# Kernel optimization log

Measured on AMD Instinct MI355X. Metric: run time of the kernel, lower is better.

Reference implementation:

```python
import jax, jax.numpy as jnp
import numpy as np
import math

EPS_NORM = 1e-12   # F.normalize eps
EPS_LN = 1e-5      # F.layer_norm default eps
EPS_STD = 1e-6     # hierarchical_norm spatial eps


def _l2_normalize(x, axis):
    n = jnp.linalg.norm(x, axis=axis, keepdims=True)
    return x / jnp.maximum(n, EPS_NORM)


def setup_inputs() -> dict:
    key = jax.random.key(0)
    k1, k2, k3, k4, k5 = jax.random.split(key, 5)
    B, C, H, W, D, L = 512, 256, 14, 14, 512, 196
    return {
        "image_features": jax.random.normal(k1, (B, D), jnp.float32),
        "text_features": jax.random.normal(k2, (B, D), jnp.float32),
        "sam_features": jax.random.normal(k3, (B, C, H, W), jnp.float32),
        "W_sim": jax.random.normal(k4, (L, D), jnp.float32) * 0.02,
        "b_sim": jax.random.normal(k5, (L,), jnp.float32) * 0.02,
    }


def reference(image_features, text_features, sam_features, W_sim, b_sim):
    B, C, H, W = sam_features.shape
    L = H * W

    # L2 normalize CLIP features
    imf = _l2_normalize(image_features, axis=1)   # (B, 512)
    txt = _l2_normalize(text_features, axis=1)    # (B, 512)

    # dynamic_similarity
    cross_attn = jnp.einsum('bc,bc->b', imf, txt)                 # (B,)
    spatial_weights = jax.nn.sigmoid(imf @ W_sim.T + b_sim)       # (B, L)
    similarity_weights = cross_attn[:, None] * spatial_weights / 10.0  # (B, L)

    # spatial self-attention over SAM features
    sam_flat = sam_features.reshape(B, C, L)                      # (B, C, L)
    sam_norm = _l2_normalize(sam_flat, axis=1)
    scores = jnp.einsum('bcl,bcm->blm', sam_norm, sam_norm) / math.sqrt(C)
    attn = jax.nn.softmax(scores, axis=-1)                        # (B, L, L)
    weighted = jnp.einsum('bcl,blm->bcm', sam_flat, attn)         # (B, C, L)

    combined = (sam_flat + weighted) * 0.5
    guide = combined * similarity_weights[:, None, :]             # (B, C, L)
    x = guide.reshape(B, C, H, W)

    # hierarchical_norm: LayerNorm over channel dim (no affine), then spatial standardization
    mu_c = x.mean(axis=1, keepdims=True)
    var_c = x.var(axis=1, keepdims=True)  # biased, matches F.layer_norm
    x = (x - mu_c) / jnp.sqrt(var_c + EPS_LN)
    sp_mean = x.mean(axis=(2, 3), keepdims=True)
    sp_std = jnp.std(x, axis=(2, 3), keepdims=True, ddof=1)  # torch .std() uses Bessel correction
    return (x - sp_mean) / (sp_std + EPS_STD)
```

## Files before the change

### kernel.cpp

```cpp
#include <hip/hip_runtime.h>
#include <math.h>


typedef float f32x4 __attribute__((ext_vector_type(4)));
typedef short s16x8 __attribute__((ext_vector_type(8)));

__device__ __forceinline__ float wsum(float v) {
#pragma unroll
  for (int o = 32; o > 0; o >>= 1) v += __shfl_xor(v, o, 64);
  return v;
}

__device__ __forceinline__ unsigned short f2bf(float f) {
  unsigned int u = __float_as_uint(f);
  u += 0x7FFFu + ((u >> 16) & 1u);
  return (unsigned short)(u >> 16);
}

__device__ __forceinline__ s16x8 pack8(f32x4 lo, f32x4 hi) {
  s16x8 r;
  r[0] = (short)f2bf(lo[0]);
  r[1] = (short)f2bf(lo[1]);
  r[2] = (short)f2bf(lo[2]);
  r[3] = (short)f2bf(lo[3]);
  r[4] = (short)f2bf(hi[0]);
  r[5] = (short)f2bf(hi[1]);
  r[6] = (short)f2bf(hi[2]);
  r[7] = (short)f2bf(hi[3]);
  return r;
}

__global__ __launch_bounds__(256) void k_simw(const float* __restrict__ img,
                                              const float* __restrict__ txt,
                                              const float* __restrict__ Wsim,
                                              const float* __restrict__ bsim,
                                              float* __restrict__ simw) {
  const int b = blockIdx.x, tid = threadIdx.x, lane = tid & 63, wv = tid >> 6;
  __shared__ float s_img[512];
  __shared__ float s_part[3][4];

  float i0 = img[b * 512 + tid], i1 = img[b * 512 + 256 + tid];
  float t0 = txt[b * 512 + tid], t1 = txt[b * 512 + 256 + tid];
  float ssi = wsum(i0 * i0 + i1 * i1);
  float sst = wsum(t0 * t0 + t1 * t1);
  float dd = wsum(i0 * t0 + i1 * t1);
  if (lane == 0) { s_part[0][wv] = ssi; s_part[1][wv] = sst; s_part[2][wv] = dd; }
  __syncthreads();
  float ni = fmaxf(sqrtf(s_part[0][0] + s_part[0][1] + s_part[0][2] + s_part[0][3]), 1e-12f);
  float nt = fmaxf(sqrtf(s_part[1][0] + s_part[1][1] + s_part[1][2] + s_part[1][3]), 1e-12f);
  float dot = s_part[2][0] + s_part[2][1] + s_part[2][2] + s_part[2][3];
  float cross = dot / (ni * nt);
  float rni = 1.0f / ni;
  s_img[tid] = i0 * rni;
  s_img[tid + 256] = i1 * rni;
  __syncthreads();

  for (int l = wv; l < 196; l += 4) {
    const float* wr = Wsim + (size_t)l * 512;
    float p = 0.f;
#pragma unroll
    for (int k = 0; k < 8; ++k) p = fmaf(s_img[lane + 64 * k], wr[lane + 64 * k], p);
    p = wsum(p);
    if (lane == 0) {
      float z = p + bsim[l];
      float sg = 1.0f / (1.0f + __expf(-z));
      simw[b * 196 + l] = cross * sg * 0.1f;
    }
  }
}

__global__ __launch_bounds__(256) void k_prep(const float* __restrict__ sam,
                                              unsigned short* __restrict__ samnT) {
  const int b = blockIdx.x, tid = threadIdx.x, lane = tid & 63, wv = tid >> 6;
  const float* __restrict__ S = sam + (size_t)b * 50176;
  unsigned short* __restrict__ NT = samnT + (size_t)b * (208 * 256);
  __shared__ float s_inv[196];
  __shared__ float T[64 * 197];

  if (tid < 196) {
    float ss = 0.f;
    for (int c = 0; c < 256; ++c) {
      float v = S[c * 196 + tid];
      ss = fmaf(v, v, ss);
    }
    s_inv[tid] = 1.0f / fmaxf(sqrtf(ss), 1e-12f);
  }
  for (int i = tid; i < 1536; i += 256) ((unsigned int*)(NT + 196 * 256))[i] = 0;
  __syncthreads();

  for (int c0 = 0; c0 < 256; c0 += 64) {
    for (int cr = wv; cr < 64; cr += 4) {
      const float* Sr = S + (c0 + cr) * 196;
      float* Tr = T + cr * 197;
      Tr[lane] = Sr[lane] * s_inv[lane];
      Tr[lane + 64] = Sr[lane + 64] * s_inv[lane + 64];
      Tr[lane + 128] = Sr[lane + 128] * s_inv[lane + 128];
      if (lane < 4) Tr[lane + 192] = Sr[lane + 192] * s_inv[lane + 192];
    }
    __syncthreads();
    const int lrow = tid >> 3, cch = tid & 7;
    for (int l0 = 0; l0 < 196; l0 += 32) {
      int l = l0 + lrow;
      if (l < 196) {
        const float* Tc = T + (cch * 8) * 197 + l;
        unsigned short r[8];
#pragma unroll
        for (int k = 0; k < 8; ++k) r[k] = f2bf(Tc[k * 197]);
        uint4 o;
        o.x = r[0] | ((unsigned int)r[1] << 16);
        o.y = r[2] | ((unsigned int)r[3] << 16);
        o.z = r[4] | ((unsigned int)r[5] << 16);
        o.w = r[6] | ((unsigned int)r[7] << 16);
        *(uint4*)(NT + l * 256 + c0 + cch * 8) = o;
      }
    }
    __syncthreads();
  }
}

__device__ __forceinline__ void proc_strip(int s, f32x4* sc, unsigned short* AT,
                                           int quad, int l15) {
  const bool mval12 = (192 + l15) < 196;
  float mx[4], rs[4];
#pragma unroll
  for (int r = 0; r < 4; ++r) {
    float m = -3e38f;
#pragma unroll
    for (int j = 0; j < 13; ++j) {
      float v = sc[j][r];
      if (j == 12 && !mval12) v = -3e38f;
      m = fmaxf(m, v);
    }
#pragma unroll
    for (int o = 1; o < 16; o <<= 1) m = fmaxf(m, __shfl_xor(m, o, 64));
    float s_ = 0.f;
#pragma unroll
    for (int j = 0; j < 13; ++j) {
      float e = __expf(sc[j][r] - m);
      if (j == 12 && !mval12) e = 0.f;
      s_ += e;
    }
#pragma unroll
    for (int o = 1; o < 16; o <<= 1) s_ += __shfl_xor(s_, o, 64);
    mx[r] = m;
    rs[r] = 1.0f / s_;
  }
  const int lb = s * 16 + quad * 4;
#pragma unroll
  for (int j = 0; j < 13; ++j) {
    unsigned short u[4];
#pragma unroll
    for (int r = 0; r < 4; ++r) {
      float a = __expf(sc[j][r] - mx[r]) * rs[r];
      if (lb + r >= 196) a = 0.f;
      u[r] = f2bf(a);
    }
    uint2 o2;
    o2.x = u[0] | ((unsigned int)u[1] << 16);
    o2.y = u[2] | ((unsigned int)u[3] << 16);
    *(uint2*)(AT + (j * 16 + l15) * 224 + lb) = o2;
  }
}

__global__ __launch_bounds__(256, 2) void k_scores(const unsigned short* __restrict__ samnT,
                                                   unsigned short* __restrict__ attnT) {
  const int b = blockIdx.x, tid = threadIdx.x, lane = tid & 63, wv = tid >> 6;
  const int quad = lane >> 4, l15 = lane & 15;
  const unsigned short* __restrict__ NT = samnT + (size_t)b * (208 * 256);
  unsigned short* __restrict__ AT = attnT + (size_t)b * (208 * 224);
  __shared__ unsigned short sN[208 * 136];

  for (int i = tid; i < 208 * 8; i += 256) {
    int m = i >> 3, k = i & 7;
    ((unsigned int*)(AT + m * 224 + 208))[k] = 0;
  }

  for (int pr = 0; pr < 2; ++pr) {
    const int p = wv + 4 * pr;
    const int s0 = 2 * p, s1 = (2 * p + 1 < 13) ? (2 * p + 1) : 12;
    f32x4 sc0[13], sc1[13];
    const f32x4 z = {0.f, 0.f, 0.f, 0.f};
#pragma unroll
    for (int j = 0; j < 13; ++j) { sc0[j] = z; sc1[j] = z; }
    for (int h = 0; h < 2; ++h) {
      __syncthreads();
      for (int i = tid; i < 208 * 16; i += 256) {
        int l = i >> 4, cc = i & 15;
        *(uint4*)(sN + l * 136 + cc * 8) = *(const uint4*)(NT + l * 256 + h * 128 + cc * 8);
      }
      __syncthreads();
      if (p < 7) {
        s16x8 A0[4], A1[4];
#pragma unroll
        for (int ct = 0; ct < 4; ++ct) {
          A0[ct] = *(const s16x8*)(sN + (s0 * 16 + l15) * 136 + ct * 32 + quad * 8);
          A1[ct] = *(const s16x8*)(sN + (s1 * 16 + l15) * 136 + ct * 32 + quad * 8);
        }
#pragma unroll
        for (int j = 0; j < 13; ++j) {
#pragma unroll
          for (int ct = 0; ct < 4; ++ct) {
            s16x8 Bf = *(const s16x8*)(sN + (j * 16 + l15) * 136 + ct * 32 + quad * 8);
            sc0[j] = __builtin_amdgcn_mfma_f32_16x16x32_bf16(A0[ct], Bf, sc0[j], 0, 0, 0);
            sc1[j] = __builtin_amdgcn_mfma_f32_16x16x32_bf16(A1[ct], Bf, sc1[j], 0, 0, 0);
          }
        }
      }
    }
    if (p < 7) {
      proc_strip(s0, sc0, AT, quad, l15);
      proc_strip(s1, sc1, AT, quad, l15);
    }
  }
}

__global__ __launch_bounds__(256, 4) void k_weighted2(const float* __restrict__ sam,
                                                      const unsigned short* __restrict__ attnT,
                                                      const float* __restrict__ simw,
                                                      float* __restrict__ out) {
  const int b = blockIdx.x, q = blockIdx.y;
  const int tid = threadIdx.x, lane = tid & 63, wv = tid >> 6;
  const int quad = lane >> 4, l15 = lane & 15;
  const float* __restrict__ S = sam + (size_t)b * 50176;
  const unsigned short* __restrict__ AT = attnT + (size_t)b * (208 * 224);
  float* __restrict__ O = out + (size_t)b * 50176;
  const int cbase = q * 64 + wv * 16;

  __shared__ float tile[4][8 * 196];

  f32x4 acc[13];
  const f32x4 z4 = {0.f, 0.f, 0.f, 0.f};
#pragma unroll
  for (int mb = 0; mb < 13; ++mb) acc[mb] = z4;

  const float* __restrict__ Sa = S + (size_t)(cbase + l15) * 196;
  const unsigned short* __restrict__ Bp = AT + l15 * 224 + quad * 8;

#pragma unroll
  for (int kt = 0; kt < 7; ++kt) {
    s16x8 A;
    if (kt < 6) {
      const float* p = Sa + kt * 32 + quad * 8;
      A = pack8(*(const f32x4*)p, *(const f32x4*)(p + 4));
    } else {
      f32x4 lo = z4;
      if (quad == 0) lo = *(const f32x4*)(Sa + 192);
      A = pack8(lo, z4);
    }
    const unsigned short* Bk = Bp + kt * 32;
#pragma unroll
    for (int mb = 0; mb < 13; ++mb) {
      s16x8 Bf = *(const s16x8*)(Bk + mb * 16 * 224);
      acc[mb] = __builtin_amdgcn_mfma_f32_16x16x32_bf16(A, Bf, acc[mb], 0, 0, 0);
    }
  }

  float wj0 = simw[b * 196 + lane] * 0.5f;
  float wj1 = simw[b * 196 + 64 + lane] * 0.5f;
  float wj2 = simw[b * 196 + 128 + lane] * 0.5f;
  float wj3 = 0.f;
  if (lane < 4) wj3 = simw[b * 196 + 192 + lane] * 0.5f;

  float* tl = &tile[wv][0];
  for (int half = 0; half < 2; ++half) {
    if ((quad >> 1) == half) {
      const int qq = quad & 1;
#pragma unroll
      for (int mb = 0; mb < 13; ++mb) {
        const int m = mb * 16 + l15;
        if (m < 196) {
#pragma unroll
          for (int r = 0; r < 4; ++r) tl[(qq * 4 + r) * 196 + m] = acc[mb][r];
        }
      }
    }
    __syncthreads();
    const int rowg0 = cbase + half * 8;
#pragma unroll
    for (int rr = 0; rr < 8; ++rr) {
      const float* trow = tl + rr * 196;
      const float* Sr = S + (size_t)(rowg0 + rr) * 196;
      float* Or = O + (size_t)(rowg0 + rr) * 196;
      Or[lane] = (Sr[lane] + trow[lane]) * wj0;
      Or[lane + 64] = (Sr[lane + 64] + trow[lane + 64]) * wj1;
      Or[lane + 128] = (Sr[lane + 128] + trow[lane + 128]) * wj2;
      if (lane < 4) Or[lane + 192] = (Sr[lane + 192] + trow[lane + 192]) * wj3;
    }
    __syncthreads();
  }
}

__global__ __launch_bounds__(256) void k_attn(const float* __restrict__ sam,
                                              const float* __restrict__ simw,
                                              float* __restrict__ out) {
  const int b = blockIdx.x;
  const int tid = threadIdx.x, lane = tid & 63, wv = tid >> 6;
  const float* __restrict__ S = sam + (size_t)b * (256 * 196);
  float* __restrict__ O = out + (size_t)b * (256 * 196);
  const float* __restrict__ SW = simw + b * 196;

  __shared__ float s_inv[196];
  __shared__ float s_max[196];
  __shared__ float s_rsum[196];
  __shared__ float bufS[28 * 197];
  __shared__ float bufT[256 * 29];

  for (int l = tid; l < 196; l += 256) {
    float ss = 0.f;
    for (int c = 0; c < 256; ++c) {
      float v = S[c * 196 + l];
      ss = fmaf(v, v, ss);
    }
    s_inv[l] = 1.0f / fmaxf(sqrtf(ss), 1e-12f);
  }

  for (int r0 = 0; r0 < 196; r0 += 28) {
    float acc[7][4];
#pragma unroll
    for (int i = 0; i < 7; ++i)
#pragma unroll
      for (int j = 0; j < 4; ++j) acc[i][j] = 0.f;
    const int lr = r0 + wv * 7;
    for (int ct = 0; ct < 8; ++ct) {
      __syncthreads();
      for (int i = tid; i < 32 * 196; i += 256)
        bufT[(i / 196) * 197 + (i % 196)] = S[ct * 32 * 196 + i];
      __syncthreads();
#pragma unroll 2
      for (int c = 0; c < 32; ++c) {
        const float* row = bufT + c * 197;
        float a[7];
#pragma unroll
        for (int i = 0; i < 7; ++i) a[i] = row[lr + i];
        float b0 = row[lane], b1 = row[lane + 64], b2 = row[lane + 128];
        float b3 = row[lane + 192];
#pragma unroll
        for (int i = 0; i < 7; ++i) {
          acc[i][0] = fmaf(a[i], b0, acc[i][0]);
          acc[i][1] = fmaf(a[i], b1, acc[i][1]);
          acc[i][2] = fmaf(a[i], b2, acc[i][2]);
          acc[i][3] = fmaf(a[i], b3, acc[i][3]);
        }
      }
    }
#pragma unroll
    for (int j = 0; j < 4; ++j) {
      int m = lane + 64 * j;
      if (m < 196) {
        float im = s_inv[m] * 0.0625f;
#pragma unroll
        for (int i = 0; i < 7; ++i)
          bufS[(wv * 7 + i) * 197 + m] = acc[i][j] * s_inv[lr + i] * im;
      }
    }
    __syncthreads();
#pragma unroll
    for (int i = 0; i < 7; ++i) {
      const int rl = wv * 7 + i;
      const float* sr = bufS + rl * 197;
      float v0 = sr[lane], v1 = sr[lane + 64], v2 = sr[lane + 128];
      bool g = (lane + 192) < 196;
      float v3 = g ? sr[lane + 192] : -1e30f;
      float mxv = fmaxf(fmaxf(v0, v1), fmaxf(v2, v3));
#pragma unroll
      for (int o = 32; o > 0; o >>= 1) mxv = fmaxf(mxv, __shfl_xor(mxv, o, 64));
      float sm = __expf(v0 - mxv) + __expf(v1 - mxv) + __expf(v2 - mxv) +
                 (g ? __expf(v3 - mxv) : 0.f);
      sm = wsum(sm);
      if (lane == 0) { s_max[r0 + rl] = mxv; s_rsum[r0 + rl] = 1.0f / sm; }
    }
  }
  __syncthreads();

  const int cg = tid >> 2, tq = tid & 3;
  for (int m0 = 0; m0 < 196; m0 += 28) {
    float acc[7][4];
#pragma unroll
    for (int i = 0; i < 7; ++i)
#pragma unroll
      for (int j = 0; j < 4; ++j) acc[i][j] = 0.f;
    const int mg = m0 + wv * 7;
    for (int ct = 0; ct < 8; ++ct) {
      __syncthreads();
      for (int i = tid; i < 32 * 196; i += 256)
        bufT[(i / 196) * 197 + (i % 196)] = S[ct * 32 * 196 + i];
      __syncthreads();
#pragma unroll 2
      for (int c = 0; c < 32; ++c) {
        const float* row = bufT + c * 197;
        float a[7];
#pragma unroll
        for (int i = 0; i < 7; ++i) a[i] = row[mg + i];
        float b0 = row[lane], b1 = row[lane + 64], b2 = row[lane + 128];
        float b3 = row[lane + 192];
#pragma unroll
        for (int i = 0; i < 7; ++i) {
          acc[i][0] = fmaf(a[i], b0, acc[i][0]);
          acc[i][1] = fmaf(a[i], b1, acc[i][1]);
          acc[i][2] = fmaf(a[i], b2, acc[i][2]);
          acc[i][3] = fmaf(a[i], b3, acc[i][3]);
        }
      }
    }
    __syncthreads();
#pragma unroll
    for (int j = 0; j < 4; ++j) {
      int l = lane + 64 * j;
      if (l < 196) {
        float il = s_inv[l] * 0.0625f;
        float mxl = s_max[l], rsl = s_rsum[l];
#pragma unroll
        for (int i = 0; i < 7; ++i) {
          float sc = acc[i][j] * s_inv[mg + i] * il;
          bufS[(wv * 7 + i) * 197 + l] = __expf(sc - mxl) * rsl;
        }
      }
    }
    __syncthreads();
    float w[4][7];
#pragma unroll
    for (int ii = 0; ii < 4; ++ii)
#pragma unroll
      for (int i = 0; i < 7; ++i) w[ii][i] = 0.f;
    for (int lt = 0; lt < 7; ++lt) {
      __syncthreads();
      for (int i = tid; i < 256 * 28; i += 256) {
        int c = i / 28, j = i - c * 28;
        bufT[c * 29 + j] = S[c * 196 + lt * 28 + j];
      }
      __syncthreads();
#pragma unroll 4
      for (int j = 0; j < 28; ++j) {
        float a0 = bufT[(cg * 4 + 0) * 29 + j];
        float a1 = bufT[(cg * 4 + 1) * 29 + j];
        float a2 = bufT[(cg * 4 + 2) * 29 + j];
        float a3 = bufT[(cg * 4 + 3) * 29 + j];
#pragma unroll
        for (int i = 0; i < 7; ++i) {
          float bv = bufS[(tq * 7 + i) * 197 + lt * 28 + j];
          w[0][i] = fmaf(a0, bv, w[0][i]);
          w[1][i] = fmaf(a1, bv, w[1][i]);
          w[2][i] = fmaf(a2, bv, w[2][i]);
          w[3][i] = fmaf(a3, bv, w[3][i]);
        }
      }
    }
#pragma unroll
    for (int i = 0; i < 7; ++i) {
      const int m = m0 + tq * 7 + i;
      float sw = SW[m] * 0.5f;
#pragma unroll
      for (int ii = 0; ii < 4; ++ii) {
        const int c = cg * 4 + ii;
        O[c * 196 + m] = (S[c * 196 + m] + w[ii][i]) * sw;
      }
    }
  }
}

__global__ __launch_bounds__(256) void k_norm(float* __restrict__ x) {
  const int b = blockIdx.x, tid = threadIdx.x;
  float* __restrict__ X = x + (size_t)b * (256 * 196);
  __shared__ float s_mu[196], s_rs[196];
  __shared__ float s_rm[256], s_rc[256];
  __shared__ float tile[256 * 29];

  if (tid < 196) {
    float s = 0.f, q = 0.f;
    for (int c = 0; c < 256; ++c) {
      float v = X[c * 196 + tid];
      s += v;
      q = fmaf(v, v, q);
    }
    float mu = s * (1.0f / 256.0f);
    float var = q * (1.0f / 256.0f) - mu * mu;
    s_mu[tid] = mu;
    s_rs[tid] = rsqrtf(fmaxf(var, 0.f) + 1e-5f);
  }
  __syncthreads();

  float rs = 0.f, rq = 0.f;
  for (int m0 = 0; m0 < 196; m0 += 28) {
    __syncthreads();
    for (int i = tid; i < 256 * 28; i += 256) {
      int c = i / 28, j = i - c * 28;
      tile[c * 29 + j] = X[c * 196 + m0 + j];
    }
    __syncthreads();
#pragma unroll
    for (int j = 0; j < 28; ++j) {
      float y = (tile[tid * 29 + j] - s_mu[m0 + j]) * s_rs[m0 + j];
      rs += y;
      rq = fmaf(y, y, rq);
    }
  }
  float rm = rs * (1.0f / 196.0f);
  float var = (rq - 196.0f * rm * rm) * (1.0f / 195.0f);
  float sd = sqrtf(fmaxf(var, 0.f));
  s_rm[tid] = rm;
  s_rc[tid] = 1.0f / (sd + 1e-6f);
  __syncthreads();

  for (int i = tid; i < 256 * 196; i += 256) {
    int c = i / 196, m = i - c * 196;
    float y = (X[i] - s_mu[m]) * s_rs[m];
    X[i] = (y - s_rm[c]) * s_rc[c];
  }
}

extern "C" void kernel_launch(void* const* d_in, const int* in_sizes, int n_in,
                              void* d_out, int out_size, void* d_ws, size_t ws_size,
                              hipStream_t stream) {
  const float* img = (const float*)d_in[0];
  const float* txt = (const float*)d_in[1];
  const float* sam = (const float*)d_in[2];
  const float* Wsim = (const float*)d_in[3];
  const float* bsim = (const float*)d_in[4];
  float* out = (float*)d_out;

  const int B = in_sizes[0] / 512;

  const size_t simw_bytes = (((size_t)B * 196 * 4) + 511) & ~(size_t)511;
  const size_t samnT_bytes = (size_t)B * 208 * 256 * 2;
  const size_t attnT_bytes = (size_t)B * 208 * 224 * 2;
  const size_t need = simw_bytes + samnT_bytes + attnT_bytes;

  float* simw = (float*)d_ws;

  k_simw<<<B, 256, 0, stream>>>(img, txt, Wsim, bsim, simw);

  if (ws_size >= need) {
    unsigned short* samnT = (unsigned short*)((char*)d_ws + simw_bytes);
    unsigned short* attnT = (unsigned short*)((char*)d_ws + simw_bytes + samnT_bytes);
    k_prep<<<B, 256, 0, stream>>>(sam, samnT);
    k_scores<<<B, 256, 0, stream>>>(samnT, attnT);
    k_weighted2<<<dim3(B, 4), 256, 0, stream>>>(sam, attnT, simw, out);
  } else {
    k_attn<<<B, 256, 0, stream>>>(sam, simw, out);
  }
  k_norm<<<B, 256, 0, stream>>>(out);
}
```

Baseline: 471.6 us.

## Split score kernel into per-strip wavefront blocks and fuse channel stats into weighted pass

Replaces the block-per-batch score kernel with one 64-thread block per 16-row strip. These blocks read operands straight from global memory (L2-friendly, XCD-aware ordering) instead of staging through LDS with barriers. The weighted kernel now also produces per-position channel sums and sums of squares, so the new normalization kernel skips one statistics pass over the output and splits each batch across two blocks. Padding zeroing moves into the prep kernel. Risks include more redundant global/L2 reads of B operands and single-pass variance precision.

```diff
diff --git a/kernel.cpp b/kernel.cpp
--- a/kernel.cpp
+++ b/kernel.cpp
@@ -70,12 +70,19 @@
 }
 
 __global__ __launch_bounds__(256) void k_prep(const float* __restrict__ sam,
-                                              unsigned short* __restrict__ samnT) {
+                                              unsigned short* __restrict__ samnT,
+                                              unsigned short* __restrict__ attnT) {
   const int b = blockIdx.x, tid = threadIdx.x, lane = tid & 63, wv = tid >> 6;
   const float* __restrict__ S = sam + (size_t)b * 50176;
   unsigned short* __restrict__ NT = samnT + (size_t)b * (208 * 256);
+  unsigned short* __restrict__ ATz = attnT + (size_t)b * (208 * 224);
   __shared__ float s_inv[196];
   __shared__ float T[64 * 197];
+
+  for (int i = tid; i < 208 * 8; i += 256) {
+    int m = i >> 3, k = i & 7;
+    ((unsigned int*)(ATz + m * 224 + 208))[k] = 0;
+  }
 
   if (tid < 196) {
     float ss = 0.f;
@@ -162,62 +169,51 @@
   }
 }
 
-__global__ __launch_bounds__(256, 2) void k_scores(const unsigned short* __restrict__ samnT,
-                                                   unsigned short* __restrict__ attnT) {
-  const int b = blockIdx.x, tid = threadIdx.x, lane = tid & 63, wv = tid >> 6;
-  const int quad = lane >> 4, l15 = lane & 15;
+__global__ __launch_bounds__(64) void k_scores2(const unsigned short* __restrict__ samnT,
+                                                unsigned short* __restrict__ attnT) {
+  int id = blockIdx.x;
+  int b, s;
+  if (gridDim.x == 512 * 13) {
+    int x = id & 7, j = id >> 3;
+    int bb = j / 13;
+    b = x * 64 + bb;
+    s = j - bb * 13;
+  } else {
+    int bb = id / 13;
+    b = bb;
+    s = id - bb * 13;
+  }
+  const int lane = threadIdx.x, quad = lane >> 4, l15 = lane & 15;
   const unsigned short* __restrict__ NT = samnT + (size_t)b * (208 * 256);
   unsigned short* __restrict__ AT = attnT + (size_t)b * (208 * 224);
-  __shared__ unsigned short sN[208 * 136];
-
-  for (int i = tid; i < 208 * 8; i += 256) {
-    int m = i >> 3, k = i & 7;
-    ((unsigned int*)(AT + m * 224 + 208))[k] = 0;
-  }
-
-  for (int pr = 0; pr < 2; ++pr) {
-    const int p = wv + 4 * pr;
-    const int s0 = 2 * p, s1 = (2 * p + 1 < 13) ? (2 * p + 1) : 12;
-    f32x4 sc0[13], sc1[13];
-    const f32x4 z = {0.f, 0.f, 0.f, 0.f};
-#pragma unroll
-    for (int j = 0; j < 13; ++j) { sc0[j] = z; sc1[j] = z; }
-    for (int h = 0; h < 2; ++h) {
-      __syncthreads();
-      for (int i = tid; i < 208 * 16; i += 256) {
-        int l = i >> 4, cc = i & 15;
-        *(uint4*)(sN + l * 136 + cc * 8) = *(const uint4*)(NT + l * 256 + h * 128 + cc * 8);
-      }
-      __syncthreads();
-      if (p < 7) {
-        s16x8 A0[4], A1[4];
-#pragma unroll
-        for (int ct = 0; ct < 4; ++ct) {
-          A0[ct] = *(const s16x8*)(sN + (s0 * 16 + l15) * 136 + ct * 32 + quad * 8);
-          A1[ct] = *(const s16x8*)(sN + (s1 * 16 + l15) * 136 + ct * 32 + quad * 8);
-        }
-#pragma unroll
-        for (int j = 0; j < 13; ++j) {
-#pragma unroll
-          for (int ct = 0; ct < 4; ++ct) {
-            s16x8 Bf = *(const s16x8*)(sN + (j * 16 + l15) * 136 + ct * 32 + quad * 8);
-            sc0[j] = __builtin_amdgcn_mfma_f32_16x16x32_bf16(A0[ct], Bf, sc0[j], 0, 0, 0);
-            sc1[j] = __builtin_amdgcn_mfma_f32_16x16x32_bf16(A1[ct], Bf, sc1[j], 0, 0, 0);
-          }
-        }
-      }
-    }
-    if (p < 7) {
-      proc_strip(s0, sc0, AT, quad, l15);
-      proc_strip(s1, sc1, AT, quad, l15);
-    }
-  }
+
+  s16x8 A[8];
+  const unsigned short* Ar = NT + (s * 16 + l15) * 256 + quad * 8;
+#pragma unroll
+  for (int ct = 0; ct < 8; ++ct) A[ct] = *(const s16x8*)(Ar + ct * 32);
+
+  f32x4 sc[13];
+  const f32x4 z = {0.f, 0.f, 0.f, 0.f};
+#pragma unroll
+  for (int j = 0; j < 13; ++j) sc[j] = z;
+
+#pragma unroll
+  for (int j = 0; j < 13; ++j) {
+    const unsigned short* Br = NT + (j * 16 + l15) * 256 + quad * 8;
+#pragma unroll
+    for (int ct = 0; ct < 8; ++ct) {
+      s16x8 Bf = *(const s16x8*)(Br + ct * 32);
+      sc[j] = __builtin_amdgcn_mfma_f32_16x16x32_bf16(A[ct], Bf, sc[j], 0, 0, 0);
+    }
+  }
+  proc_strip(s, sc, AT, quad, l15);
 }
 
 __global__ __launch_bounds__(256, 4) void k_weighted2(const float* __restrict__ sam,
                                                       const unsigned short* __restrict__ attnT,
                                                       const float* __restrict__ simw,
-                                                      float* __restrict__ out) {
+                                                      float* __restrict__ out,
+                                                      float* __restrict__ stats) {
   const int b = blockIdx.x, q = blockIdx.y;
   const int tid = threadIdx.x, lane = tid & 63, wv = tid >> 6;
   const int quad = lane >> 4, l15 = lane & 15;
@@ -261,6 +257,9 @@
   float wj3 = 0.f;
   if (lane < 4) wj3 = simw[b * 196 + 192 + lane] * 0.5f;
 
+  float st0 = 0.f, st1 = 0.f, st2 = 0.f, st3 = 0.f;
+  float sq0 = 0.f, sq1 = 0.f, sq2 = 0.f, sq3 = 0.f;
+
   float* tl = &tile[wv][0];
   for (int half = 0; half < 2; ++half) {
     if ((quad >> 1) == half) {
@@ -281,10 +280,82 @@
       const float* trow = tl + rr * 196;
       const float* Sr = S + (size_t)(rowg0 + rr) * 196;
       float* Or = O + (size_t)(rowg0 + rr) * 196;
-      Or[lane] = (Sr[lane] + trow[lane]) * wj0;
-      Or[lane + 64] = (Sr[lane + 64] + trow[lane + 64]) * wj1;
-      Or[lane + 128] = (Sr[lane + 128] + trow[lane + 128]) * wj2;
-      if (lane < 4) Or[lane + 192] = (Sr[lane + 192] + trow[lane + 192]) * wj3;
+      float v0 = (Sr[lane] + trow[lane]) * wj0;
+      float v1 = (Sr[lane + 64] + trow[lane + 64]) * wj1;
+      float v2 = (Sr[lane + 128] + trow[lane + 128]) * wj2;
+      Or[lane] = v0;
+      Or[lane + 64] = v1;
+      Or[lane + 128] = v2;
+      st0 += v0; sq0 = fmaf(v0, v0, sq0);
+      st1 += v1; sq1 = fmaf(v1, v1, sq1);
+      st2 += v2; sq2 = fmaf(v2, v2, sq2);
+      if (lane < 4) {
+        float v3 = (Sr[lane + 192] + trow[lane + 192]) * wj3;
+        Or[lane + 192] = v3;
+        st3 += v3; sq3 = fmaf(v3, v3, sq3);
+      }
+    }
+    __syncthreads();
+  }
+
+  tl[lane] = st0; tl[lane + 64] = st1; tl[lane + 128] = st2;
+  if (lane < 4) tl[lane + 192] = st3;
+  tl[784 + lane] = sq0; tl[784 + lane + 64] = sq1; tl[784 + lane + 128] = sq2;
+  if (lane < 4) tl[784 + lane + 192] = sq3;
+  __syncthreads();
+  if (tid < 196) {
+    float s = tile[0][tid] + tile[1][tid] + tile[2][tid] + tile[3][tid];
+    float qsum = tile[0][784 + tid] + tile[1][784 + tid] + tile[2][784 + tid] + tile[3][784 + tid];
+    stats[((size_t)(b * 4 + q) * 2 + 0) * 196 + tid] = s;
+    stats[((size_t)(b * 4 + q) * 2 + 1) * 196 + tid] = qsum;
+  }
+}
+
+__global__ __launch_bounds__(256) void k_norm2(float* __restrict__ x,
+                                               const float* __restrict__ stats) {
+  const int b = blockIdx.x, q = blockIdx.y, tid = threadIdx.x;
+  float* __restrict__ X = x + (size_t)b * 50176 + (size_t)q * 128 * 196;
+  __shared__ float s_mu[196], s_rs[196];
+  __shared__ float s_rm[32], s_rc[32];
+  __shared__ float T[32][197];
+
+  if (tid < 196) {
+    const float* st = stats + (size_t)b * 8 * 196;
+    float s = st[tid] + st[2 * 196 + tid] + st[4 * 196 + tid] + st[6 * 196 + tid];
+    float sq = st[196 + tid] + st[3 * 196 + tid] + st[5 * 196 + tid] + st[7 * 196 + tid];
+    float mu = s * (1.0f / 256.0f);
+    float var = sq * (1.0f / 256.0f) - mu * mu;
+    s_mu[tid] = mu;
+    s_rs[tid] = rsqrtf(fmaxf(var, 0.f) + 1e-5f);
+  }
+  __syncthreads();
+
+  for (int rg = 0; rg < 4; ++rg) {
+    float* Xg = X + rg * 32 * 196;
+    for (int i = tid; i < 32 * 196; i += 256) T[i / 196][i % 196] = Xg[i];
+    __syncthreads();
+    const int r = tid >> 3, p = tid & 7;
+    float ys = 0.f, yq = 0.f;
+    for (int m = p; m < 196; m += 8) {
+      float y = (T[r][m] - s_mu[m]) * s_rs[m];
+      ys += y;
+      yq = fmaf(y, y, yq);
+    }
+    ys += __shfl_xor(ys, 1, 64); yq += __shfl_xor(yq, 1, 64);
+    ys += __shfl_xor(ys, 2, 64); yq += __shfl_xor(yq, 2, 64);
+    ys += __shfl_xor(ys, 4, 64); yq += __shfl_xor(yq, 4, 64);
+    if (p == 0) {
+      float rm = ys * (1.0f / 196.0f);
+      float var = (yq - 196.0f * rm * rm) * (1.0f / 195.0f);
+      float sd = sqrtf(fmaxf(var, 0.f));
+      s_rm[r] = rm;
+      s_rc[r] = 1.0f / (sd + 1e-6f);
+    }
+    __syncthreads();
+    for (int i = tid; i < 32 * 196; i += 256) {
+      int rr = i / 196, m = i % 196;
+      float y = (T[rr][m] - s_mu[m]) * s_rs[m];
+      Xg[i] = (y - s_rm[rr]) * s_rc[rr];
     }
     __syncthreads();
   }
@@ -523,7 +594,8 @@
   const size_t simw_bytes = (((size_t)B * 196 * 4) + 511) & ~(size_t)511;
   const size_t samnT_bytes = (size_t)B * 208 * 256 * 2;
   const size_t attnT_bytes = (size_t)B * 208 * 224 * 2;
-  const size_t need = simw_bytes + samnT_bytes + attnT_bytes;
+  const size_t stats_bytes = (size_t)B * 4 * 2 * 196 * 4;
+  const size_t need = simw_bytes + samnT_bytes + attnT_bytes + stats_bytes;
 
   float* simw = (float*)d_ws;
 
@@ -532,11 +604,13 @@
   if (ws_size >= need) {
     unsigned short* samnT = (unsigned short*)((char*)d_ws + simw_bytes);
     unsigned short* attnT = (unsigned short*)((char*)d_ws + simw_bytes + samnT_bytes);
-    k_prep<<<B, 256, 0, stream>>>(sam, samnT);
-    k_scores<<<B, 256, 0, stream>>>(samnT, attnT);
-    k_weighted2<<<dim3(B, 4), 256, 0, stream>>>(sam, attnT, simw, out);
+    float* stats = (float*)((char*)d_ws + simw_bytes + samnT_bytes + attnT_bytes);
+    k_prep<<<B, 256, 0, stream>>>(sam, samnT, attnT);
+    k_scores2<<<B * 13, 64, 0, stream>>>(samnT, attnT);
+    k_weighted2<<<dim3(B, 4), 256, 0, stream>>>(sam, attnT, simw, out, stats);
+    k_norm2<<<dim3(B, 2), 256, 0, stream>>>(out, stats);
   } else {
     k_attn<<<B, 256, 0, stream>>>(sam, simw, out);
-  }
-  k_norm<<<B, 256, 0, stream>>>(out);
-}
+    k_norm<<<B, 256, 0, stream>>>(out);
+  }
+}
```

New measurement: 486.4 us. 1.03x slower.
